# Kernel optimization log

Measured on AMD Instinct MI355X. Metric: run time of the kernel, lower is better.

## Reference

```python
import jax, jax.numpy as jnp
import numpy as np

DIM = 1024
HEAD = 8
SPLIT = DIM // HEAD
EPS = 1e-6


def layernorm(x, gamma, beta):
    m = jnp.mean(x, axis=-1, keepdims=True)
    v = jnp.mean(jnp.square(x - m), axis=-1, keepdims=True)
    return (x - m) / jnp.sqrt(v + EPS) * gamma + beta


def setup_inputs() -> dict:
    key = jax.random.key(0)
    ks = jax.random.split(key, 6)
    s = 0.02
    return {
        "x": jax.random.normal(ks[0], (4, 2048, DIM), dtype=jnp.float32),
        "W_in": jax.random.normal(ks[1], (DIM, DIM), dtype=jnp.float32) * s,
        "gamma": jnp.ones((DIM,), jnp.float32),
        "beta": jnp.zeros((DIM,), jnp.float32),
        "Wq": jax.random.normal(ks[2], (HEAD, SPLIT, SPLIT), dtype=jnp.float32) * s,
        "Wk": jax.random.normal(ks[3], (HEAD, SPLIT, SPLIT), dtype=jnp.float32) * s,
        "Wv": jax.random.normal(ks[4], (HEAD, SPLIT, SPLIT), dtype=jnp.float32) * s,
        "Wf": jax.random.normal(ks[5], (DIM, DIM), dtype=jnp.float32) * s,
        "bf": jnp.zeros((DIM,), jnp.float32),
    }


def reference(x, W_in, gamma, beta, Wq, Wk, Wv, Wf, bf):
    B, S, _ = x.shape
    mod = x @ W_in  # [B,S,DIM], Dense no bias
    # pre-norm then split into heads: [B,S,HEAD,SPLIT]
    h = layernorm(mod, gamma, beta).reshape(B, S, HEAD, SPLIT)
    # per-head Q/K/V projections (batched over heads instead of Python loop)
    q = jnp.einsum('bshd,hde->bhse', h, Wq)
    k = jnp.einsum('bshd,hde->bhse', h, Wk)
    v = jnp.einsum('bshd,hde->bhse', h, Wv)
    # keras Attention(): unscaled dot-product scores (use_scale=False)
    scores = jnp.einsum('bhqe,bhke->bhqk', q, k)
    attn = jax.nn.softmax(scores, axis=-1)
    o = jnp.einsum('bhqk,bhke->bqhe', attn, v).reshape(B, S, DIM)
    mod = mod + o  # residual
    # FFN residual with shared LayerNorm params and ELU Dense
    mod = mod + jax.nn.elu(layernorm(mod, gamma, beta) @ Wf + bf)
    return mod
```

## Files before the change

### kernel.cpp

```cpp
#include <hip/hip_runtime.h>
#include <hip/hip_bf16.h>

#define DIMN 1024
#define NHEAD 8
#define ESPL 128
#define NB 4
#define SEQ 2048
#define NROWS (NB * SEQ)
#define LNEPS 1e-6f

typedef unsigned short u16;
typedef unsigned int u32;
typedef __attribute__((ext_vector_type(8))) short short8;
typedef __attribute__((ext_vector_type(4))) short s16x4;
typedef __attribute__((ext_vector_type(4))) float f32x4;

__device__ __forceinline__ u16 f2bf(float f) {
  u32 u = __float_as_uint(f);
  u += 0x7FFFu + ((u >> 16) & 1u);
  return (u16)(u >> 16);
}

__device__ __forceinline__ uint2 pack4bf(float4 v) {
  uint2 r;
  r.x = (u32)f2bf(v.x) | ((u32)f2bf(v.y) << 16);
  r.y = (u32)f2bf(v.z) | ((u32)f2bf(v.w) << 16);
  return r;
}

__device__ __forceinline__ u32 pk2bf(float a, float b) {
  return (u32)f2bf(a) | ((u32)f2bf(b) << 16);
}

__device__ __forceinline__ float eluf(float x) { return x > 0.f ? x : expm1f(x); }

__device__ __forceinline__ float redsum16(float v) {
  v += __shfl_xor(v, 1);
  v += __shfl_xor(v, 2);
  v += __shfl_xor(v, 4);
  v += __shfl_xor(v, 8);
  return v;
}

__device__ __forceinline__ void gl2lds16(const u16* g, u16* l) {
  __builtin_amdgcn_global_load_lds((const __attribute__((address_space(1))) u32*)g,
                                   (__attribute__((address_space(3))) u32*)l, 16, 0, 0);
}

__global__ __launch_bounds__(256) void conv_bf16(const float* __restrict__ src,
                                                 u16* __restrict__ dst) {
  int base = (blockIdx.x * 256 + threadIdx.x) * 4;
  *(uint2*)(dst + base) = pack4bf(*(const float4*)(src + base));
}

__global__ __launch_bounds__(256) void ln_apply(const float* __restrict__ modp,
                                                const float* __restrict__ gamma,
                                                const float* __restrict__ beta,
                                                const float* __restrict__ s1p,
                                                const float* __restrict__ s2p,
                                                u16* __restrict__ outb) {
  int base = (blockIdx.x * 256 + threadIdx.x) * 4;
  int row = base >> 10, col = base & 1023;
  float s1 = s1p[row], s2 = s2p[row];
  float mu = s1 * (1.f / DIMN);
  float rsd = rsqrtf(fmaxf(s2 * (1.f / DIMN) - mu * mu, 0.f) + LNEPS);
  float4 v = *(const float4*)(modp + base);
  float4 g = *(const float4*)(gamma + col);
  float4 bb = *(const float4*)(beta + col);
  v.x = (v.x - mu) * rsd * g.x + bb.x;
  v.y = (v.y - mu) * rsd * g.y + bb.y;
  v.z = (v.z - mu) * rsd * g.z + bb.z;
  v.w = (v.w - mu) * rsd * g.w + bb.w;
  *(uint2*)(outb + base) = pack4bf(v);
}

__device__ __forceinline__ void wtrans_body(const float* __restrict__ src,
                                            u16* __restrict__ dst, int K, int N, int n0,
                                            int k0) {
  __shared__ u16 tl[64][68];
  const int t = threadIdx.x;
  const int r = t >> 2;
#pragma unroll
  for (int j = 0; j < 4; j++) {
    int f = (t & 3) + j * 4;
    float4 v = *(const float4*)(src + (size_t)(k0 + r) * N + n0 + f * 4);
    *(uint2*)&tl[r][f * 4] = pack4bf(v);
  }
  __syncthreads();
#pragma unroll
  for (int j = 0; j < 4; j++) {
    int f = (t & 3) + j * 4;
    ushort4 o;
    o.x = tl[f * 4 + 0][r];
    o.y = tl[f * 4 + 1][r];
    o.z = tl[f * 4 + 2][r];
    o.w = tl[f * 4 + 3][r];
    *(ushort4*)(dst + (size_t)(n0 + r) * K + k0 + f * 4) = o;
  }
}

__global__ __launch_bounds__(256) void wtrans_big(const float* __restrict__ sA,
                                                  u16* __restrict__ dA,
                                                  const float* __restrict__ sB,
                                                  u16* __restrict__ dB) {
  const float* s = blockIdx.z ? sB : sA;
  u16* d = blockIdx.z ? dB : dA;
  wtrans_body(s, d, DIMN, DIMN, blockIdx.x * 64, blockIdx.y * 64);
}

__global__ __launch_bounds__(256) void wtrans_small(
    const float* __restrict__ sq, const float* __restrict__ sk, const float* __restrict__ sv,
    u16* __restrict__ dq, u16* __restrict__ dk, u16* __restrict__ dv) {
  const int mi = blockIdx.z >> 3, hh = blockIdx.z & 7;
  const float* s = (mi == 0) ? sq : (mi == 1) ? sk : sv;
  u16* d = (mi == 0) ? dq : (mi == 1) ? dk : dv;
  s += (size_t)hh * ESPL * ESPL;
  d += (size_t)hh * ESPL * ESPL;
  wtrans_body(s, d, ESPL, ESPL, blockIdx.x * 64, blockIdx.y * 64);
}

template <int MODE>
__global__ __launch_bounds__(256, 2) void gemm_bf16(
    const u16* __restrict__ A, const u16* __restrict__ Bt, const float* __restrict__ resid,
    const float* __restrict__ bias, float* __restrict__ s1p, float* __restrict__ s2p,
    float* __restrict__ C) {
  __shared__ __align__(16) char lds[65536];
  const int t = threadIdx.x;
  const int w = t >> 6, lane = t & 63, quad = lane >> 4, l16 = lane & 15;
  const int wm = w & 1, wn = w >> 1;
  const int m0 = blockIdx.y * 128, n0 = blockIdx.x * 128;

  auto stage = [&](int koff, int bi) {
    const u16* ag = A + (size_t)m0 * DIMN + koff;
    const u16* bg = Bt + (size_t)n0 * DIMN + koff;
    u16* As = (u16*)(lds + bi * 32768);
    u16* Bs = (u16*)(lds + bi * 32768 + 16384);
#pragma unroll
    for (int i = 0; i < 4; i++) {
      int pbase = (w * 4 + i) * 64;
      int p = pbase + lane;
      int r = p >> 3, c8 = (p & 7) ^ (r & 7);
      gl2lds16(ag + (size_t)r * DIMN + c8 * 8, As + pbase * 8);
      gl2lds16(bg + (size_t)r * DIMN + c8 * 8, Bs + pbase * 8);
    }
  };

  f32x4 acc[4][4];
#pragma unroll
  for (int mt = 0; mt < 4; mt++)
#pragma unroll
    for (int nt = 0; nt < 4; nt++) acc[mt][nt] = (f32x4){0.f, 0.f, 0.f, 0.f};

  stage(0, 0);
  __syncthreads();
  for (int kt = 0; kt < DIMN / 64; kt++) {
    if (kt + 1 < DIMN / 64) stage((kt + 1) * 64, (kt + 1) & 1);
    const u16* As = (const u16*)(lds + (kt & 1) * 32768);
    const u16* Bs = (const u16*)(lds + (kt & 1) * 32768 + 16384);
#pragma unroll
    for (int ks = 0; ks < 2; ks++) {
      short8 af[4], bfr[4];
#pragma unroll
      for (int mt = 0; mt < 4; mt++) {
        int row = wm * 64 + mt * 16 + l16;
        int pc = (ks * 4 + quad) ^ (row & 7);
        af[mt] = *(const short8*)(As + row * 64 + pc * 8);
      }
#pragma unroll
      for (int nt = 0; nt < 4; nt++) {
        int row = wn * 64 + nt * 16 + l16;
        int pc = (ks * 4 + quad) ^ (row & 7);
        bfr[nt] = *(const short8*)(Bs + row * 64 + pc * 8);
      }
#pragma unroll
      for (int mt = 0; mt < 4; mt++)
#pragma unroll
        for (int nt = 0; nt < 4; nt++)
          acc[mt][nt] = __builtin_amdgcn_mfma_f32_16x16x32_bf16(af[mt], bfr[nt], acc[mt][nt], 0, 0, 0);
    }
    __syncthreads();
  }
#pragma unroll
  for (int mt = 0; mt < 4; mt++) {
#pragma unroll
    for (int r = 0; r < 4; r++) {
      int row = m0 + wm * 64 + mt * 16 + quad * 4 + r;
      float s1 = 0.f, s2 = 0.f;
#pragma unroll
      for (int nt = 0; nt < 4; nt++) {
        int col = n0 + wn * 64 + nt * 16 + l16;
        size_t off = (size_t)row * DIMN + col;
        float v = acc[mt][nt][r];
        if (MODE == 0) {
          C[off] = v;
          s1 += v;
          s2 += v * v;
        } else {
          C[off] = resid[off] + eluf(v + bias[col]);
        }
      }
      if (MODE == 0) {
        s1 = redsum16(s1);
        s2 = redsum16(s2);
        if (l16 == 0) {
          atomicAdd(s1p + row, s1);
          atomicAdd(s2p + row, s2);
        }
      }
    }
  }
}

#define QP 136

__global__ __launch_bounds__(256) void qkv_mfma(
    const float* __restrict__ modp, const u16* __restrict__ wqt, const u16* __restrict__ wkt,
    const u16* __restrict__ wvt, const float* __restrict__ gamma, const float* __restrict__ beta,
    const float* __restrict__ s1p, const float* __restrict__ s2p, u16* __restrict__ qo,
    u16* __restrict__ ko, u16* __restrict__ vto) {
  __shared__ u16 Asl[128 * QP];
  __shared__ u16 Bsl[128 * QP];
  const int t = threadIdx.x;
  const int w = t >> 6, lane = t & 63, quad = lane >> 4, l16 = lane & 15;
  const int wm = w & 1, wn = w >> 1;
  const int s0 = blockIdx.x * 128;
  const int bh = blockIdx.y;
  const int b = bh >> 3, hh = bh & 7;
  const int sr8 = t >> 3, sf8 = t & 7;
#pragma unroll
  for (int p = 0; p < 4; p++) {
    int r = sr8 + 32 * p;
    int rowg = b * SEQ + s0 + r;
    float s1 = s1p[rowg], s2 = s2p[rowg];
    float mu = s1 * (1.f / DIMN);
    float rsd = rsqrtf(fmaxf(s2 * (1.f / DIMN) - mu * mu, 0.f) + LNEPS);
    const float* ap = modp + (size_t)rowg * DIMN + hh * ESPL;
#pragma unroll
    for (int j = 0; j < 4; j++) {
      int f = sf8 + j * 8;
      float4 v = *(const float4*)(ap + f * 4);
      float4 g = *(const float4*)(gamma + hh * ESPL + f * 4);
      float4 bb = *(const float4*)(beta + hh * ESPL + f * 4);
      v.x = (v.x - mu) * rsd * g.x + bb.x;
      v.y = (v.y - mu) * rsd * g.y + bb.y;
      v.z = (v.z - mu) * rsd * g.z + bb.z;
      v.w = (v.w - mu) * rsd * g.w + bb.w;
      *(uint2*)(Asl + r * QP + f * 4) = pack4bf(v);
    }
  }
  __syncthreads();
  short8 afr[4][4];
#pragma unroll
  for (int k4 = 0; k4 < 4; k4++)
#pragma unroll
    for (int mt = 0; mt < 4; mt++)
      afr[k4][mt] = *(const short8*)(Asl + (wm * 64 + mt * 16 + l16) * QP + k4 * 32 + quad * 8);

  const u16* Ws[3] = {wqt, wkt, wvt};
  for (int mi = 0; mi < 3; mi++) {
    __syncthreads();
    const u16* wsrc = Ws[mi] + ((size_t)hh << 14);
#pragma unroll
    for (int p = 0; p < 4; p++) {
      int r = sr8 + 32 * p;
#pragma unroll
      for (int j = 0; j < 2; j++) {
        int f = sf8 + j * 8;
        *(uint4*)(Bsl + r * QP + f * 8) = *(const uint4*)(wsrc + r * ESPL + f * 8);
      }
    }
    __syncthreads();
    f32x4 acc[4][4];
#pragma unroll
    for (int mt = 0; mt < 4; mt++)
#pragma unroll
      for (int nt = 0; nt < 4; nt++) acc[mt][nt] = (f32x4){0.f, 0.f, 0.f, 0.f};
#pragma unroll
    for (int k4 = 0; k4 < 4; k4++) {
      short8 bfr[4];
#pragma unroll
      for (int nt = 0; nt < 4; nt++)
        bfr[nt] = *(const short8*)(Bsl + (wn * 64 + nt * 16 + l16) * QP + k4 * 32 + quad * 8);
#pragma unroll
      for (int mt = 0; mt < 4; mt++)
#pragma unroll
        for (int nt = 0; nt < 4; nt++)
          acc[mt][nt] = __builtin_amdgcn_mfma_f32_16x16x32_bf16(afr[k4][mt], bfr[nt], acc[mt][nt], 0, 0, 0);
    }
    if (mi < 2) {
      u16* o = (mi == 0) ? qo : ko;
#pragma unroll
      for (int mt = 0; mt < 4; mt++)
#pragma unroll
        for (int r = 0; r < 4; r++) {
          int s = s0 + wm * 64 + mt * 16 + quad * 4 + r;
#pragma unroll
          for (int nt = 0; nt < 4; nt++) {
            int e = wn * 64 + nt * 16 + l16;
            o[((size_t)bh * SEQ + s) * ESPL + e] = f2bf(acc[mt][nt][r]);
          }
        }
    } else {
#pragma unroll
      for (int mt = 0; mt < 4; mt++)
#pragma unroll
        for (int nt = 0; nt < 4; nt++) {
          int e = wn * 64 + nt * 16 + l16;
          int sbase = s0 + wm * 64 + mt * 16 + quad * 4;
          ushort4 pk;
          pk.x = f2bf(acc[mt][nt][0]);
          pk.y = f2bf(acc[mt][nt][1]);
          pk.z = f2bf(acc[mt][nt][2]);
          pk.w = f2bf(acc[mt][nt][3]);
          *(ushort4*)(vto + ((size_t)bh * ESPL + e) * SEQ + sbase) = pk;
        }
    }
  }
}

#define OBP 132

__global__ __launch_bounds__(256, 2) void attn_mfma(const u16* __restrict__ q,
                                                    const u16* __restrict__ kk,
                                                    const u16* __restrict__ vt,
                                                    float* __restrict__ modp,
                                                    float* __restrict__ s1p,
                                                    float* __restrict__ s2p) {
  __shared__ __align__(16) char lds[65536];
  const int t = threadIdx.x;
  const int w = t >> 6, lane = t & 63, quad = lane >> 4, l16 = lane & 15;
  const int qt = blockIdx.x;
  const int bh = blockIdx.y;
  const int b = bh >> 3, hh = bh & 7;
  const size_t qkbase = (size_t)bh * SEQ * ESPL;
  const int qrow0 = qt * 128 + w * 32;
  const u16* kg0 = kk + qkbase;
  const u16* vg0 = vt + qkbase;

  short8 qf[2][4];
#pragma unroll
  for (int g = 0; g < 2; g++) {
    const u16* qrow = q + qkbase + (size_t)(qrow0 + g * 16 + l16) * ESPL + quad * 8;
#pragma unroll
    for (int kc = 0; kc < 4; kc++) qf[g][kc] = *(const short8*)(qrow + kc * 32);
  }

  float m_st[2] = {-1e30f, -1e30f}, l_st[2] = {0.f, 0.f};
  f32x4 oacc[2][8];
#pragma unroll
  for (int g = 0; g < 2; g++)
#pragma unroll
    for (int et = 0; et < 8; et++) oacc[g][et] = (f32x4){0.f, 0.f, 0.f, 0.f};

  auto stage = [&](int kt, int bi) {
    const u16* kg = kg0 + (size_t)kt * 64 * ESPL;
    const u16* vg = vg0 + (size_t)kt * 64;
    u16* Ksb = (u16*)(lds + bi * 32768);
    u16* Vsb = (u16*)(lds + bi * 32768 + 16384);
#pragma unroll
    for (int i = 0; i < 4; i++) {
      int pbase = w * 64 + i * 256;
      int p = pbase + lane;
      int r = p >> 4, c8 = (p & 15) ^ (r & 15);
      gl2lds16(kg + r * ESPL + c8 * 8, Ksb + pbase * 8);
      int e = p >> 3, v8 = (p & 7) ^ (e & 7);
      gl2lds16(vg + (size_t)e * SEQ + v8 * 8, Vsb + pbase * 8);
    }
  };

  stage(0, 0);
  __syncthreads();

  for (int kt = 0; kt < SEQ / 64; kt++) {
    if (kt + 1 < SEQ / 64) stage(kt + 1, (kt + 1) & 1);
    const u16* Ks = (const u16*)(lds + (kt & 1) * 32768);
    const u16* Vs = (const u16*)(lds + (kt & 1) * 32768 + 16384);
    f32x4 sacc[4][2];
#pragma unroll
    for (int mt = 0; mt < 4; mt++)
#pragma unroll
      for (int g = 0; g < 2; g++) sacc[mt][g] = (f32x4){0.f, 0.f, 0.f, 0.f};
#pragma unroll
    for (int mt = 0; mt < 4; mt++) {
#pragma unroll
      for (int kc = 0; kc < 4; kc++) {
        short8 kf = *(const short8*)(Ks + (mt * 16 + l16) * 128 + (((kc * 4 + quad) ^ l16) << 3));
        sacc[mt][0] = __builtin_amdgcn_mfma_f32_16x16x32_bf16(kf, qf[0][kc], sacc[mt][0], 0, 0, 0);
        sacc[mt][1] = __builtin_amdgcn_mfma_f32_16x16x32_bf16(kf, qf[1][kc], sacc[mt][1], 0, 0, 0);
      }
    }
    s16x4 pfrag[2][4];
    float alpha[2];
#pragma unroll
    for (int g = 0; g < 2; g++) {
      float mloc = sacc[0][g][0];
#pragma unroll
      for (int mt = 0; mt < 4; mt++)
#pragma unroll
        for (int r = 0; r < 4; r++) mloc = fmaxf(mloc, sacc[mt][g][r]);
      mloc = fmaxf(mloc, __shfl_xor(mloc, 16));
      mloc = fmaxf(mloc, __shfl_xor(mloc, 32));
      float mnew = fmaxf(m_st[g], mloc);
      alpha[g] = __expf(m_st[g] - mnew);
      m_st[g] = mnew;
      float sum = 0.f;
#pragma unroll
      for (int mt = 0; mt < 4; mt++) {
        float p0 = __expf(sacc[mt][g][0] - mnew);
        float p1 = __expf(sacc[mt][g][1] - mnew);
        float p2 = __expf(sacc[mt][g][2] - mnew);
        float p3 = __expf(sacc[mt][g][3] - mnew);
        sum += (p0 + p1) + (p2 + p3);
        union {
          s16x4 s;
          uint2 u;
        } cv;
        cv.u = make_uint2(pk2bf(p0, p1), pk2bf(p2, p3));
        pfrag[g][mt] = cv.s;
      }
      sum += __shfl_xor(sum, 16);
      sum += __shfl_xor(sum, 32);
      l_st[g] = l_st[g] * alpha[g] + sum;
    }
#pragma unroll
    for (int g = 0; g < 2; g++)
#pragma unroll
      for (int et = 0; et < 8; et++)
#pragma unroll
        for (int r = 0; r < 4; r++) oacc[g][et][r] *= alpha[g];
#pragma unroll
    for (int et = 0; et < 8; et++) {
#pragma unroll
      for (int mt = 0; mt < 4; mt++) {
        s16x4 vf = *(const s16x4*)(Vs + (size_t)(et * 16 + l16) * 64 +
                                   ((((mt * 2 + (quad >> 1)) ^ (l16 & 7)) << 3) + (quad & 1) * 4));
        oacc[0][et] = __builtin_amdgcn_mfma_f32_16x16x16bf16_1k(vf, pfrag[0][mt], oacc[0][et], 0, 0, 0);
        oacc[1][et] = __builtin_amdgcn_mfma_f32_16x16x16bf16_1k(vf, pfrag[1][mt], oacc[1][et], 0, 0, 0);
      }
    }
    __syncthreads();
  }

  float* Obuf = (float*)lds;
  const int rr = t >> 3, cc = (t & 7) << 4;
  for (int c = 0; c < 4; c++) {
    if (w == c) {
      float linv[2] = {1.f / l_st[0], 1.f / l_st[1]};
#pragma unroll
      for (int g = 0; g < 2; g++)
#pragma unroll
        for (int et = 0; et < 8; et++) {
          f32x4 ov = oacc[g][et];
          ov[0] *= linv[g];
          ov[1] *= linv[g];
          ov[2] *= linv[g];
          ov[3] *= linv[g];
          *(f32x4*)(Obuf + (size_t)(g * 16 + l16) * OBP + et * 16 + quad * 4) = ov;
        }
    }
    __syncthreads();
    int qglob = qt * 128 + c * 32 + rr;
    float* mp = modp + ((size_t)(b * SEQ + qglob)) * DIMN + hh * ESPL + cc;
    float s1 = 0.f, s2 = 0.f;
#pragma unroll
    for (int j = 0; j < 4; j++) {
      float4 ov = *(const float4*)(Obuf + (size_t)rr * OBP + cc + j * 4);
      float4 mv = *(const float4*)(mp + j * 4);
      mv.x += ov.x;
      mv.y += ov.y;
      mv.z += ov.z;
      mv.w += ov.w;
      *(float4*)(mp + j * 4) = mv;
      s1 += (mv.x + mv.y) + (mv.z + mv.w);
      s2 += (mv.x * mv.x + mv.y * mv.y) + (mv.z * mv.z + mv.w * mv.w);
    }
    s1 += __shfl_xor(s1, 1);
    s1 += __shfl_xor(s1, 2);
    s1 += __shfl_xor(s1, 4);
    s2 += __shfl_xor(s2, 1);
    s2 += __shfl_xor(s2, 2);
    s2 += __shfl_xor(s2, 4);
    if ((t & 7) == 0) {
      atomicAdd(s1p + b * SEQ + qglob, s1);
      atomicAdd(s2p + b * SEQ + qglob, s2);
    }
    __syncthreads();
  }
}

extern "C" void kernel_launch(void* const* d_in, const int* in_sizes, int n_in, void* d_out,
                              int out_size, void* d_ws, size_t ws_size, hipStream_t stream) {
  (void)in_sizes;
  (void)n_in;
  (void)out_size;
  (void)ws_size;
  const float* x = (const float*)d_in[0];
  const float* W_in = (const float*)d_in[1];
  const float* gamma = (const float*)d_in[2];
  const float* beta = (const float*)d_in[3];
  const float* Wq = (const float*)d_in[4];
  const float* Wk = (const float*)d_in[5];
  const float* Wv = (const float*)d_in[6];
  const float* Wf = (const float*)d_in[7];
  const float* bf = (const float*)d_in[8];
  float* out = (float*)d_out;

  char* ws = (char*)d_ws;
  const size_t MB = 1024ull * 1024;
  float* mod = (float*)ws;
  u16* qb = (u16*)(ws + 32 * MB);
  u16* kb = (u16*)(ws + 48 * MB);
  u16* vtb = (u16*)(ws + 64 * MB);
  float* sums = (float*)(ws + 80 * MB);
  float* s1a = sums;
  float* s2a = s1a + NROWS;
  float* s1b = s2a + NROWS;
  float* s2b = s1b + NROWS;
  u16* wqt = (u16*)(ws + 80 * MB + 4 * NROWS * sizeof(float));
  u16* wkt = wqt + NHEAD * ESPL * ESPL;
  u16* wvt = wkt + NHEAD * ESPL * ESPL;
  u16* wt2 = wvt + NHEAD * ESPL * ESPL;
  u16* wt1 = qb;
  u16* xb = kb;
  u16* modb = qb;

  hipMemsetAsync(sums, 0, 4 * NROWS * sizeof(float), stream);
  conv_bf16<<<NROWS * DIMN / 1024, 256, 0, stream>>>(x, xb);
  wtrans_big<<<dim3(16, 16, 2), 256, 0, stream>>>(W_in, wt1, Wf, wt2);
  wtrans_small<<<dim3(2, 2, 24), 256, 0, stream>>>(Wq, Wk, Wv, wqt, wkt, wvt);

  dim3 gg(DIMN / 128, NROWS / 128);
  gemm_bf16<0><<<gg, 256, 0, stream>>>(xb, wt1, nullptr, nullptr, s1a, s2a, mod);
  qkv_mfma<<<dim3(SEQ / 128, NB * NHEAD), 256, 0, stream>>>(mod, wqt, wkt, wvt, gamma, beta,
                                                            s1a, s2a, qb, kb, vtb);
  attn_mfma<<<dim3(SEQ / 128, NB * NHEAD), 256, 0, stream>>>(qb, kb, vtb, mod, s1b, s2b);
  ln_apply<<<NROWS * DIMN / 1024, 256, 0, stream>>>(mod, gamma, beta, s1b, s2b, modb);
  gemm_bf16<1><<<gg, 256, 0, stream>>>(modb, wt2, mod, bf, nullptr, nullptr, out);
}
```

Baseline: 318.9 us.

## Use hardware bf16 pack, lazy softmax rescale, and MFMA priority hints in attention

Replaces the software round-to-nearest bf16 conversion with the v_cvt_pk_bf16_f32 instruction for packing pairs. In the flash-attention loop, the running max and output accumulator are now rescaled only when a wave's new tile max exceeds the stored max by more than a threshold, which skips most per-tile multiplies of the output accumulator. It also flattens the max reduction into a tree and wraps the MFMA blocks with s_setprio to favour matrix issue across waves. The lazy rescale lets exponentials reach up to e^8 before renormalising, which the fp32 accumulators can absorb.

```diff
diff --git a/kernel.cpp b/kernel.cpp
--- a/kernel.cpp
+++ b/kernel.cpp
@@ -21,15 +21,17 @@
   return (u16)(u >> 16);
 }
 
+__device__ __forceinline__ u32 pk2bf(float a, float b) {
+  u32 r;
+  asm("v_cvt_pk_bf16_f32 %0, %1, %2" : "=v"(r) : "v"(a), "v"(b));
+  return r;
+}
+
 __device__ __forceinline__ uint2 pack4bf(float4 v) {
   uint2 r;
-  r.x = (u32)f2bf(v.x) | ((u32)f2bf(v.y) << 16);
-  r.y = (u32)f2bf(v.z) | ((u32)f2bf(v.w) << 16);
+  r.x = pk2bf(v.x, v.y);
+  r.y = pk2bf(v.z, v.w);
   return r;
-}
-
-__device__ __forceinline__ u32 pk2bf(float a, float b) {
-  return (u32)f2bf(a) | ((u32)f2bf(b) << 16);
 }
 
 __device__ __forceinline__ float eluf(float x) { return x > 0.f ? x : expm1f(x); }
@@ -307,18 +309,17 @@
         for (int nt = 0; nt < 4; nt++) {
           int e = wn * 64 + nt * 16 + l16;
           int sbase = s0 + wm * 64 + mt * 16 + quad * 4;
-          ushort4 pk;
-          pk.x = f2bf(acc[mt][nt][0]);
-          pk.y = f2bf(acc[mt][nt][1]);
-          pk.z = f2bf(acc[mt][nt][2]);
-          pk.w = f2bf(acc[mt][nt][3]);
-          *(ushort4*)(vto + ((size_t)bh * ESPL + e) * SEQ + sbase) = pk;
+          uint2 pk;
+          pk.x = pk2bf(acc[mt][nt][0], acc[mt][nt][1]);
+          pk.y = pk2bf(acc[mt][nt][2], acc[mt][nt][3]);
+          *(uint2*)(vto + ((size_t)bh * ESPL + e) * SEQ + sbase) = pk;
         }
     }
   }
 }
 
 #define OBP 132
+#define RESCALE_THR 8.f
 
 __global__ __launch_bounds__(256, 2) void attn_mfma(const u16* __restrict__ q,
                                                     const u16* __restrict__ kk,
@@ -380,6 +381,7 @@
     for (int mt = 0; mt < 4; mt++)
 #pragma unroll
       for (int g = 0; g < 2; g++) sacc[mt][g] = (f32x4){0.f, 0.f, 0.f, 0.f};
+    __builtin_amdgcn_s_setprio(1);
 #pragma unroll
     for (int mt = 0; mt < 4; mt++) {
 #pragma unroll
@@ -389,27 +391,37 @@
         sacc[mt][1] = __builtin_amdgcn_mfma_f32_16x16x32_bf16(kf, qf[1][kc], sacc[mt][1], 0, 0, 0);
       }
     }
+    __builtin_amdgcn_s_setprio(0);
     s16x4 pfrag[2][4];
     float alpha[2];
+    bool updf[2];
 #pragma unroll
     for (int g = 0; g < 2; g++) {
-      float mloc = sacc[0][g][0];
-#pragma unroll
-      for (int mt = 0; mt < 4; mt++)
-#pragma unroll
-        for (int r = 0; r < 4; r++) mloc = fmaxf(mloc, sacc[mt][g][r]);
+      const f32x4 a = sacc[0][g], b2 = sacc[1][g], c2 = sacc[2][g], d2 = sacc[3][g];
+      float t0 = fmaxf(fmaxf(a[0], a[1]), a[2]);
+      float t1 = fmaxf(fmaxf(a[3], b2[0]), b2[1]);
+      float t2 = fmaxf(fmaxf(b2[2], b2[3]), c2[0]);
+      float t3 = fmaxf(fmaxf(c2[1], c2[2]), c2[3]);
+      float t4 = fmaxf(fmaxf(d2[0], d2[1]), d2[2]);
+      float mloc = fmaxf(fmaxf(fmaxf(t0, t1), t2), fmaxf(fmaxf(t3, t4), d2[3]));
       mloc = fmaxf(mloc, __shfl_xor(mloc, 16));
       mloc = fmaxf(mloc, __shfl_xor(mloc, 32));
-      float mnew = fmaxf(m_st[g], mloc);
-      alpha[g] = __expf(m_st[g] - mnew);
-      m_st[g] = mnew;
+      updf[g] = !__all(mloc - m_st[g] <= RESCALE_THR);
+      if (updf[g]) {
+        float mnew = fmaxf(m_st[g], mloc);
+        alpha[g] = __expf(m_st[g] - mnew);
+        m_st[g] = mnew;
+      } else {
+        alpha[g] = 1.f;
+      }
+      const float mk = m_st[g];
       float sum = 0.f;
 #pragma unroll
       for (int mt = 0; mt < 4; mt++) {
-        float p0 = __expf(sacc[mt][g][0] - mnew);
-        float p1 = __expf(sacc[mt][g][1] - mnew);
-        float p2 = __expf(sacc[mt][g][2] - mnew);
-        float p3 = __expf(sacc[mt][g][3] - mnew);
+        float p0 = __expf(sacc[mt][g][0] - mk);
+        float p1 = __expf(sacc[mt][g][1] - mk);
+        float p2 = __expf(sacc[mt][g][2] - mk);
+        float p3 = __expf(sacc[mt][g][3] - mk);
         sum += (p0 + p1) + (p2 + p3);
         union {
           s16x4 s;
@@ -422,12 +434,19 @@
       sum += __shfl_xor(sum, 32);
       l_st[g] = l_st[g] * alpha[g] + sum;
     }
-#pragma unroll
-    for (int g = 0; g < 2; g++)
+    if (updf[0]) {
 #pragma unroll
       for (int et = 0; et < 8; et++)
 #pragma unroll
-        for (int r = 0; r < 4; r++) oacc[g][et][r] *= alpha[g];
+        for (int r = 0; r < 4; r++) oacc[0][et][r] *= alpha[0];
+    }
+    if (updf[1]) {
+#pragma unroll
+      for (int et = 0; et < 8; et++)
+#pragma unroll
+        for (int r = 0; r < 4; r++) oacc[1][et][r] *= alpha[1];
+    }
+    __builtin_amdgcn_s_setprio(1);
 #pragma unroll
     for (int et = 0; et < 8; et++) {
 #pragma unroll
@@ -438,6 +457,7 @@
         oacc[1][et] = __builtin_amdgcn_mfma_f32_16x16x16bf16_1k(vf, pfrag[1][mt], oacc[1][et], 0, 0, 0);
       }
     }
+    __builtin_amdgcn_s_setprio(0);
     __syncthreads();
   }
 
```

Result: faster. 308.7 us (-3.2%).
